# Optimization experiments

Hardware: AMD Instinct MI355X
Metric: run time of the kernel (lower is better)

Reference implementation:

```python
import jax, jax.numpy as jnp
import numpy as np

TOPK = 2

def setup_inputs() -> dict:
    key = jax.random.key(0)
    ks = jax.random.split(key, 5)
    B, S, D, H, E = 2, 4096, 1024, 2048, 8
    x = jax.random.normal(ks[0], (B, S, D), dtype=jnp.float32)
    router_w = jax.random.normal(ks[1], (E, D), dtype=jnp.float32) * 0.02
    w1 = jax.random.normal(ks[2], (E, D, H), dtype=jnp.float32) * 0.02
    w3 = jax.random.normal(ks[3], (E, D, H), dtype=jnp.float32) * 0.02
    w2 = jax.random.normal(ks[4], (E, H, D), dtype=jnp.float32) * 0.02
    return {"x": x, "router_w": router_w, "w1": w1, "w3": w3, "w2": w2}

def reference(x, router_w, w1, w3, w2):
    B, S, D = x.shape
    E = router_w.shape[0]
    xf = x.reshape(-1, D)                      # [T, D]
    T = xf.shape[0]
    logits = (xf @ router_w.T).astype(jnp.float32)      # [T, E]
    weights, indices = jax.lax.top_k(logits, TOPK)      # [T, k]
    weights = jax.nn.softmax(weights, axis=-1).astype(x.dtype)
    prob = jax.nn.softmax(logits, axis=-1)              # [T, E] fp32
    P = prob.mean(axis=0).astype(x.dtype)               # [E]
    mask = jnp.zeros((T, E), jnp.float32).at[jnp.arange(T)[:, None], indices].set(1.0)
    f = mask.mean(axis=0).astype(x.dtype)               # [E]
    aux_loss = E * jnp.sum(f * P)
    out = jnp.zeros_like(xf)
    for e in range(E):
        # combine weight for expert e per token (0 if not routed here)
        coef = jnp.sum(jnp.where(indices == e, weights, jnp.zeros_like(weights)), axis=-1)  # [T]
        h = jax.nn.silu(xf @ w1[e]) * (xf @ w3[e])      # [T, H] SwiGLU
        out = out + coef[:, None] * (h @ w2[e])         # masked combine == gather/scatter
    return out.reshape(B, S, D), aux_loss
```

## Files before the change

### kernel.cpp

```cpp
#include <hip/hip_runtime.h>
#include <hip/hip_bf16.h>

#define TT 8192
#define DD 1024
#define HH 2048
#define EE 8

typedef __bf16 bf16x8 __attribute__((ext_vector_type(8)));
typedef float floatx4 __attribute__((ext_vector_type(4)));
typedef short shortx8 __attribute__((ext_vector_type(8)));

__device__ __forceinline__ short f2bf(float f) {
  unsigned u = __float_as_uint(f);
  u += 0x7fffu + ((u >> 16) & 1u);
  return (short)(u >> 16);
}

__device__ __forceinline__ float bf2f(short s) {
  return __uint_as_float(((unsigned)(unsigned short)s) << 16);
}

__device__ __forceinline__ void gld16(const void* g, void* l) {
  __builtin_amdgcn_global_load_lds((const __attribute__((address_space(1))) void*)g,
                                   (__attribute__((address_space(3))) void*)l, 16, 0, 0);
}

__global__ __launch_bounds__(256) void prep_kernel(
    const float* __restrict__ x, const float* __restrict__ rw,
    const float* __restrict__ w1, const float* __restrict__ w3, const float* __restrict__ w2,
    int* __restrict__ cpad, float* __restrict__ ppad, int* __restrict__ ctr,
    int* __restrict__ offsets, float* __restrict__ out_aux,
    int* __restrict__ list_token, float* __restrict__ list_coef,
    int* __restrict__ tokpk, float* __restrict__ tokcf,
    short* __restrict__ xb, short* __restrict__ w13t, short* __restrict__ w2t)
{
  __shared__ short T[64 * 74];
  __shared__ int   sE0[32], sE1[32], lcnt[EE], sbase[EE], lp0[32], lp1[32];
  __shared__ float sG0[32], sG1[32], sP[EE];
  const int b = blockIdx.x;
  const int tid = threadIdx.x;

  if (b < 256) {
    if (tid < EE) { sP[tid] = 0.f; lcnt[tid] = 0; }
    __syncthreads();
    const int lane = tid & 63, wv = tid >> 6;
    const int t0 = b * 32;
    for (int ti = 0; ti < 8; ++ti) {
      const int s = wv * 8 + ti;
      const int t = t0 + s;
      float sc[EE];
#pragma unroll
      for (int e = 0; e < EE; ++e) sc[e] = 0.f;
#pragma unroll
      for (int j = 0; j < 4; ++j) {
        float4 xv = *(const float4*)(x + (size_t)t * DD + j * 256 + lane * 4);
#pragma unroll
        for (int e = 0; e < EE; ++e) {
          float4 rv = *(const float4*)(rw + e * DD + j * 256 + lane * 4);
          sc[e] += xv.x * rv.x + xv.y * rv.y + xv.z * rv.z + xv.w * rv.w;
        }
        if (xb) {
          short4 sv = make_short4(f2bf(xv.x), f2bf(xv.y), f2bf(xv.z), f2bf(xv.w));
          *(short4*)(xb + (size_t)t * DD + j * 256 + lane * 4) = sv;
        }
      }
#pragma unroll
      for (int off = 32; off > 0; off >>= 1)
#pragma unroll
        for (int e = 0; e < EE; ++e)
          sc[e] += __shfl_down(sc[e], off);
      if (lane == 0) {
        int i0 = 0; float l0 = sc[0];
        for (int e = 1; e < EE; ++e) if (sc[e] > l0) { l0 = sc[e]; i0 = e; }
        int i1 = -1; float l1 = -3.4e38f;
        for (int e = 0; e < EE; ++e) if (e != i0 && sc[e] > l1) { l1 = sc[e]; i1 = e; }
        const float g0 = 1.f / (1.f + __expf(l1 - l0));
        float pr[EE]; float sum = 0.f;
        for (int e = 0; e < EE; ++e) { pr[e] = __expf(sc[e] - l0); sum += pr[e]; }
        const float inv = 1.f / sum;
        for (int e = 0; e < EE; ++e) atomicAdd(&sP[e], pr[e] * inv);
        sE0[s] = i0; sE1[s] = i1; sG0[s] = g0; sG1[s] = 1.f - g0;
      }
    }
    __syncthreads();
    if (tid < 32) {
      lp0[tid] = atomicAdd(&lcnt[sE0[tid]], 1);
      lp1[tid] = atomicAdd(&lcnt[sE1[tid]], 1);
    }
    __syncthreads();
    if (tid < EE) {
      sbase[tid] = atomicAdd(&cpad[tid * 16], lcnt[tid]);
      atomicAdd(&ppad[tid * 16], sP[tid]);
    }
    __syncthreads();
    if (tid < 32) {
      int e0 = sE0[tid], e1 = sE1[tid], t = t0 + tid;
      int p0 = sbase[e0] + lp0[tid];
      int p1 = sbase[e1] + lp1[tid];
      list_token[e0 * TT + p0] = t; list_coef[e0 * TT + p0] = sG0[tid];
      list_token[e1 * TT + p1] = t; list_coef[e1 * TT + p1] = sG1[tid];
      tokpk[t * 2]     = (e0 << 13) | p0;  tokcf[t * 2]     = sG0[tid];
      tokpk[t * 2 + 1] = (e1 << 13) | p1;  tokcf[t * 2 + 1] = sG1[tid];
    }
    __syncthreads();
    if (tid == 0) {
      __threadfence();
      if (atomicAdd(ctr, 1) == 255) {
        float aux = 0.f; int off = 0;
        for (int e = 0; e < EE; ++e) {
          int c   = atomicAdd(&cpad[e * 16], 0);
          float p = atomicAdd(&ppad[e * 16], 0.f);
          aux += ((float)c / (float)TT) * (p / (float)TT);
          offsets[e] = off; off += c;
        }
        *out_aux = aux * (float)EE;
      }
    }
  } else if (b < 256 + 8192) {
    const int u = b - 256;
    const int xx = u & 31, yy = (u >> 5) & 15, z = u >> 9;
    const int is3 = (z >= EE) ? 1 : 0;
    const int e = is3 ? (z - EE) : z;
    const float* in = (is3 ? w3 : w1) + (size_t)e * DD * HH;
    short* o = w13t + (size_t)e * DD * HH * 2;
    const int c0 = xx * 64, r0 = yy * 64;
#pragma unroll
    for (int p = 0; p < 4; ++p) {
      int r = p * 16 + (tid >> 4), c4 = (tid & 15) * 4;
      float4 v = *(const float4*)(in + (size_t)(r0 + r) * HH + c0 + c4);
      short4 s = make_short4(f2bf(v.x), f2bf(v.y), f2bf(v.z), f2bf(v.w));
      *(short4*)&T[r * 74 + c4] = s;
    }
    __syncthreads();
#pragma unroll
    for (int q = 0; q < 2; ++q) {
      int uu = q * 256 + tid;
      int oc = uu >> 3, k8 = (uu & 7) * 8;
      shortx8 s;
#pragma unroll
      for (int j = 0; j < 8; ++j) s[j] = T[(k8 + j) * 74 + oc];
      int c = c0 + oc;
      int grow = 2 * (c & ~31) + (c & 31) + (is3 ? 32 : 0);
      *(shortx8*)&o[(size_t)grow * DD + r0 + k8] = s;
    }
  } else {
    const int v = b - 256 - 8192;
    const int xx = v & 15, yy = (v >> 4) & 31, z = v >> 9;
    const float* in = w2 + (size_t)z * HH * DD;
    short* o = w2t + (size_t)z * HH * DD;
    const int c0 = xx * 64, r0 = yy * 64;
#pragma unroll
    for (int p = 0; p < 4; ++p) {
      int r = p * 16 + (tid >> 4), c4 = (tid & 15) * 4;
      float4 vv = *(const float4*)(in + (size_t)(r0 + r) * DD + c0 + c4);
      short4 s = make_short4(f2bf(vv.x), f2bf(vv.y), f2bf(vv.z), f2bf(vv.w));
      *(short4*)&T[r * 74 + c4] = s;
    }
    __syncthreads();
#pragma unroll
    for (int q = 0; q < 2; ++q) {
      int uu = q * 256 + tid;
      int oc = uu >> 3, k8 = (uu & 7) * 8;
      shortx8 s;
#pragma unroll
      for (int j = 0; j < 8; ++j) s[j] = T[(k8 + j) * 74 + oc];
      *(shortx8*)&o[(size_t)(c0 + oc) * HH + r0 + k8] = s;
    }
  }
}

__global__ __launch_bounds__(256) void convt_kernel(const float* __restrict__ in, short* __restrict__ out,
                                                    int R, int C)
{
  __shared__ short T[64 * 74];
  const int t = threadIdx.x;
  in  += (size_t)blockIdx.z * R * C;
  out += (size_t)blockIdx.z * R * C;
  const int c0 = blockIdx.x * 64, r0 = blockIdx.y * 64;
#pragma unroll
  for (int p = 0; p < 4; ++p) {
    int r = p * 16 + (t >> 4), c4 = (t & 15) * 4;
    float4 v = *(const float4*)(in + (size_t)(r0 + r) * C + c0 + c4);
    short4 s = make_short4(f2bf(v.x), f2bf(v.y), f2bf(v.z), f2bf(v.w));
    *(short4*)&T[r * 74 + c4] = s;
  }
  __syncthreads();
#pragma unroll
  for (int q = 0; q < 2; ++q) {
    int u = q * 256 + t;
    int oc = u >> 3, k8 = (u & 7) * 8;
    shortx8 s;
#pragma unroll
    for (int j = 0; j < 8; ++j) s[j] = T[(k8 + j) * 74 + oc];
    *(shortx8*)&out[(size_t)(c0 + oc) * R + r0 + k8] = s;
  }
}


#define PH_BAR()  { __builtin_amdgcn_s_barrier(); __builtin_amdgcn_sched_barrier(0); }
#define WAITL0()  { asm volatile("s_waitcnt lgkmcnt(0)" ::: "memory"); __builtin_amdgcn_sched_barrier(0); }
#define WAITVN(n) { asm volatile("s_waitcnt vmcnt(" #n ")" ::: "memory"); __builtin_amdgcn_sched_barrier(0); }

template<int NT>
__device__ __forceinline__ void mma_core(char* SM, int tid,
    const char* a00, const char* a01, const char* a10, const char* a11,
    const char* b00, const char* b01, const char* b10, const char* b11,
    floatx4 (&acc)[8][4])
{
  const int lane = tid & 63, w = tid >> 6;
  const int l16 = lane & 15, quad = lane >> 4;
  const int wm = (w >> 2) & 1, wn = w & 3;
  const int cx = (((l16 >> 1) & 1) << 4) | (((l16 >> 2) & 1) << 5) | ((l16 & 1) << 6);
  const int ck0 = (quad * 16) ^ cx;
  const int arb = (wm * 128 + l16) * 128;
  const int brb = 32768 + (wn * 64 + l16) * 128;
  const int wq = w * 2048;

#define SA_(u,h,p0,p1) { gld16((p0) + (size_t)(u) * 128, SM + (((u) & 1) << 16) + (h) * 16384 + wq); \
                         gld16((p1) + (size_t)(u) * 128, SM + (((u) & 1) << 16) + (h) * 16384 + wq + 1024); }
#define SB_(u,h,p0,p1) { gld16((p0) + (size_t)(u) * 128, SM + (((u) & 1) << 16) + 32768 + (h) * 16384 + wq); \
                         gld16((p1) + (size_t)(u) * 128, SM + (((u) & 1) << 16) + 32768 + (h) * 16384 + wq + 1024); }
#define LA_(mi) { a[mi][0] = *(const bf16x8*)(SM + cur + arb + (mi) * 2048 + ck0); \
                  a[mi][1] = *(const bf16x8*)(SM + cur + arb + (mi) * 2048 + (ck0 ^ 64)); }
#define LB_(ni) { b[ni][0] = *(const bf16x8*)(SM + cur + brb + (ni) * 2048 + ck0); \
                  b[ni][1] = *(const bf16x8*)(SM + cur + brb + (ni) * 2048 + (ck0 ^ 64)); }
#define MM_(mi,ni) { acc[mi][ni] = __builtin_amdgcn_mfma_f32_16x16x32_bf16(a[mi][0], b[ni][0], acc[mi][ni], 0, 0, 0); \
                     acc[mi][ni] = __builtin_amdgcn_mfma_f32_16x16x32_bf16(a[mi][1], b[ni][1], acc[mi][ni], 0, 0, 0); }

  SA_(0, 0, a00, a01); SA_(0, 1, a10, a11);
  SB_(0, 0, b00, b01); SB_(0, 1, b10, b11);
  SA_(1, 0, a00, a01); SA_(1, 1, a10, a11);
  WAITVN(4);
  __builtin_amdgcn_s_barrier();
  __builtin_amdgcn_sched_barrier(0);

#pragma unroll 2
  for (int t = 0; t < NT; ++t) {
    const int cur = (t & 1) << 16;
    bf16x8 a[8][2], b[4][2];
    LA_(0) LA_(1) LA_(2) LA_(3) LB_(0) LB_(1)
    if (t + 1 < NT) SB_(t + 1, 0, b00, b01);
    PH_BAR(); WAITL0();
    __builtin_amdgcn_s_setprio(1);
    MM_(0,0) MM_(1,0) MM_(2,0) MM_(3,0) MM_(0,1) MM_(1,1) MM_(2,1) MM_(3,1)
    __builtin_amdgcn_s_setprio(0);
    PH_BAR();
    LA_(4) LA_(5) LA_(6) LA_(7) LB_(2) LB_(3)
    if (t + 1 < NT) SB_(t + 1, 1, b10, b11);
    PH_BAR(); WAITL0();
    __builtin_amdgcn_s_setprio(1);
    MM_(4,2) MM_(5,2) MM_(6,2) MM_(7,2) MM_(4,3) MM_(5,3) MM_(6,3) MM_(7,3)
    __builtin_amdgcn_s_setprio(0);
    PH_BAR();
    if (t + 2 < NT) SA_(t + 2, 0, a00, a01);
    PH_BAR();
    __builtin_amdgcn_s_setprio(1);
    MM_(0,2) MM_(1,2) MM_(2,2) MM_(3,2) MM_(0,3) MM_(1,3) MM_(2,3) MM_(3,3)
    __builtin_amdgcn_s_setprio(0);
    PH_BAR();
    if (t + 2 < NT) SA_(t + 2, 1, a10, a11);
    PH_BAR();
    __builtin_amdgcn_s_setprio(1);
    MM_(4,0) MM_(5,0) MM_(6,0) MM_(7,0) MM_(4,1) MM_(5,1) MM_(6,1) MM_(7,1)
    __builtin_amdgcn_s_setprio(0);
    if (t + 2 < NT) { WAITVN(4); } else { WAITVN(0); }
    PH_BAR();
  }
#undef SA_
#undef SB_
#undef LA_
#undef LB_
#undef MM_
}

__global__ __launch_bounds__(512, 2) void g1p_kernel(
    const short* __restrict__ xb, const short* __restrict__ w13t,
    const int* __restrict__ cpad, const int* __restrict__ offsets,
    const int* __restrict__ list_token, short* __restrict__ Hbuf)
{
  const int lin = blockIdx.x + 16 * (blockIdx.y + 32 * blockIdx.z);
  const int xcd = lin & 7, c = lin >> 3;
  const int e = c >> 6, rb = (c >> 1) & 31, nb = (xcd << 1) | (c & 1);
  const int cnt = cpad[e * 16];
  if (rb * 256 >= cnt) return;
  __shared__ char SM[131072];
  const int tid = threadIdx.x;
  const int lane = tid & 63, w = tid >> 6;
  const int srow = lane >> 3;
  const int scol = (((lane ^ (lane >> 4)) & 1) << 4)
                 | ((((lane >> 1) ^ (lane >> 5)) & 1) << 5)
                 | ((((lane >> 2) ^ (lane >> 3)) & 1) << 6);
  const int* lt = list_token + e * TT;
  const char* ap[2][2];
#pragma unroll
  for (int h = 0; h < 2; ++h)
#pragma unroll
    for (int i = 0; i < 2; ++i) {
      int gr = rb * 256 + h * 128 + (w * 2 + i) * 8 + srow;
      int tok = (gr < cnt) ? lt[gr] : lt[0];
      ap[h][i] = (const char*)xb + (size_t)tok * 2048 + scol;
    }
  const char* bb = (const char*)w13t + ((size_t)e * 4096 + nb * 256) * 2048
                 + (size_t)(w * 16 + srow) * 2048 + scol;
  floatx4 acc[8][4] = {};
  mma_core<16>(SM, tid, ap[0][0], ap[0][1], ap[1][0], ap[1][1],
               bb, bb + 8 * 2048, bb + 128 * 2048, bb + 136 * 2048, acc);
  const int off = offsets[e];
  const int l16 = lane & 15, quad = lane >> 4;
  const int wm = (w >> 2) & 1, wn = w & 3;
#pragma unroll
  for (int mi = 0; mi < 8; ++mi)
#pragma unroll
    for (int r = 0; r < 4; ++r) {
      int grow = rb * 256 + wm * 128 + mi * 16 + quad * 4 + r;
      if (grow < cnt) {
        size_t rowbase = (size_t)(off + grow) * HH + nb * 128 + wn * 32;
#pragma unroll
        for (int ni = 0; ni < 2; ++ni) {
          float aa = acc[mi][ni][r], bbv = acc[mi][ni + 2][r];
          float hv = aa / (1.f + __expf(-aa)) * bbv;
          Hbuf[rowbase + ni * 16 + l16] = f2bf(hv);
        }
      }
    }
}

__global__ __launch_bounds__(512, 2) void g2q_kernel(
    const short* __restrict__ Hbuf, const short* __restrict__ w2t,
    const int* __restrict__ cpad, const int* __restrict__ offsets,
    short* __restrict__ Obuf)
{
  const int nb = blockIdx.x, rb = blockIdx.y, e = blockIdx.z;
  const int cnt = cpad[e * 16];
  if (rb * 256 >= cnt) return;
  __shared__ char SM[131072];
  const int tid = threadIdx.x;
  const int lane = tid & 63, w = tid >> 6;
  const int srow = lane >> 3;
  const int scol = (((lane ^ (lane >> 4)) & 1) << 4)
                 | ((((lane >> 1) ^ (lane >> 5)) & 1) << 5)
                 | ((((lane >> 2) ^ (lane >> 3)) & 1) << 6);
  const int off = offsets[e];
  const char* ap[2][2];
#pragma unroll
  for (int h = 0; h < 2; ++h)
#pragma unroll
    for (int i = 0; i < 2; ++i) {
      int gr = rb * 256 + h * 128 + (w * 2 + i) * 8 + srow;
      int cg = (gr < cnt) ? gr : (cnt - 1);
      ap[h][i] = (const char*)Hbuf + (size_t)(off + cg) * 4096 + scol;
    }
  const char* bb = (const char*)w2t + ((size_t)e * DD + nb * 256) * 4096
                 + (size_t)(w * 16 + srow) * 4096 + scol;
  floatx4 acc[8][4] = {};
  mma_core<32>(SM, tid, ap[0][0], ap[0][1], ap[1][0], ap[1][1],
               bb, bb + 8 * 4096, bb + 128 * 4096, bb + 136 * 4096, acc);
  const int l16 = lane & 15, quad = lane >> 4;
  const int wm = (w >> 2) & 1, wn = w & 3;
#pragma unroll
  for (int mi = 0; mi < 8; ++mi)
#pragma unroll
    for (int r = 0; r < 4; ++r) {
      int grow = rb * 256 + wm * 128 + mi * 16 + quad * 4 + r;
      if (grow < cnt) {
        short* orow = Obuf + (size_t)(off + grow) * DD + nb * 256 + wn * 64;
#pragma unroll
        for (int ni = 0; ni < 4; ++ni)
          orow[ni * 16 + l16] = f2bf(acc[mi][ni][r]);
      }
    }
}

__global__ __launch_bounds__(256) void combine_kernel(
    const short* __restrict__ Obuf, const int* __restrict__ offsets,
    const int* __restrict__ tokpk, const float* __restrict__ tokcf,
    float* __restrict__ out)
{
  const int tid = threadIdx.x, lane = tid & 63, wv = tid >> 6;
  const int t = blockIdx.x * 4 + wv;
  const int pk0 = tokpk[t * 2], pk1 = tokpk[t * 2 + 1];
  const float c0 = tokcf[t * 2], c1 = tokcf[t * 2 + 1];
  const size_t r0 = (size_t)(offsets[pk0 >> 13] + (pk0 & 8191)) * DD;
  const size_t r1 = (size_t)(offsets[pk1 >> 13] + (pk1 & 8191)) * DD;
  float* orow = out + (size_t)t * DD;
#pragma unroll
  for (int p = 0; p < 2; ++p) {
    int cidx = p * 512 + lane * 8;
    shortx8 a = *(const shortx8*)(Obuf + r0 + cidx);
    shortx8 b = *(const shortx8*)(Obuf + r1 + cidx);
    float v[8];
#pragma unroll
    for (int j = 0; j < 8; ++j) v[j] = c0 * bf2f(a[j]) + c1 * bf2f(b[j]);
    *(float4*)(orow + cidx)     = make_float4(v[0], v[1], v[2], v[3]);
    *(float4*)(orow + cidx + 4) = make_float4(v[4], v[5], v[6], v[7]);
  }
}

__global__ __launch_bounds__(256, 2) void g1s_kernel(
    const float* __restrict__ x, const float* __restrict__ w1, const float* __restrict__ w3,
    const int* __restrict__ cpad, const int* __restrict__ offsets,
    const int* __restrict__ list_token, short* __restrict__ Hbuf)
{
  const int e = blockIdx.z, rb = blockIdx.y, nb = blockIdx.x;
  const int cnt = cpad[e * 16];
  if (rb * 128 >= cnt) return;
  __shared__ short Asm[128 * 40];
  __shared__ short B1sm[128 * 40];
  __shared__ short B3sm[128 * 40];
  const int tid = threadIdx.x, lane = tid & 63, wv = tid >> 6;
  const int wm = (wv >> 1) * 64, wn = (wv & 1) * 64;
  const int quad = lane >> 4, l16 = lane & 15;
  floatx4 acc1[4][4] = {{{0.f}}};
  floatx4 acc3[4][4] = {{{0.f}}};
  const int ar = tid >> 3, ak = (tid & 7) * 4;
  const int bp = tid & 63, bq = tid >> 6;
  const int bswz = (bq ^ ((bp >> 2) & 3)) * 8;
  const int bo0 = (2 * bp) * 40 + bswz, bo1 = bo0 + 40;
  int aro[4], bro[4];
#pragma unroll
  for (int mi = 0; mi < 4; ++mi) aro[mi] = (wm + mi * 16 + l16) * 40 + quad * 8;
#pragma unroll
  for (int ni = 0; ni < 4; ++ni) {
    int nl = wn + ni * 16 + l16;
    bro[ni] = nl * 40 + ((quad ^ ((nl >> 3) & 3)) * 8);
  }
  int tok[4];
#pragma unroll
  for (int i = 0; i < 4; ++i) {
    int gr = rb * 128 + ar + 32 * i;
    tok[i] = (gr < cnt) ? list_token[e * TT + gr] : list_token[e * TT];
  }
  const float* w1e = w1 + (size_t)e * DD * HH + (size_t)nb * 128;
  const float* w3e = w3 + (size_t)e * DD * HH + (size_t)nb * 128;
  for (int k0 = 0; k0 < DD; k0 += 32) {
    __syncthreads();
#pragma unroll
    for (int i = 0; i < 4; ++i) {
      int r = ar + 32 * i;
      float4 v = *(const float4*)(x + (size_t)tok[i] * DD + k0 + ak);
      short4 sv = make_short4(f2bf(v.x), f2bf(v.y), f2bf(v.z), f2bf(v.w));
      *(short4*)&Asm[r * 40 + ak] = sv;
    }
    {
      float2 u[8];
#pragma unroll
      for (int j = 0; j < 8; ++j) u[j] = *(const float2*)(w1e + (size_t)(k0 + bq * 8 + j) * HH + 2 * bp);
      shortx8 p0, p1;
#pragma unroll
      for (int j = 0; j < 8; ++j) { p0[j] = f2bf(u[j].x); p1[j] = f2bf(u[j].y); }
      *(shortx8*)&B1sm[bo0] = p0; *(shortx8*)&B1sm[bo1] = p1;
    }
    {
      float2 u[8];
#pragma unroll
      for (int j = 0; j < 8; ++j) u[j] = *(const float2*)(w3e + (size_t)(k0 + bq * 8 + j) * HH + 2 * bp);
      shortx8 p0, p1;
#pragma unroll
      for (int j = 0; j < 8; ++j) { p0[j] = f2bf(u[j].x); p1[j] = f2bf(u[j].y); }
      *(shortx8*)&B3sm[bo0] = p0; *(shortx8*)&B3sm[bo1] = p1;
    }
    __syncthreads();
    bf16x8 af[4], b1f[4], b3f[4];
#pragma unroll
    for (int mi = 0; mi < 4; ++mi) af[mi] = *(const bf16x8*)&Asm[aro[mi]];
#pragma unroll
    for (int ni = 0; ni < 4; ++ni) {
      b1f[ni] = *(const bf16x8*)&B1sm[bro[ni]];
      b3f[ni] = *(const bf16x8*)&B3sm[bro[ni]];
    }
#pragma unroll
    for (int mi = 0; mi < 4; ++mi)
#pragma unroll
      for (int ni = 0; ni < 4; ++ni) {
        acc1[mi][ni] = __builtin_amdgcn_mfma_f32_16x16x32_bf16(af[mi], b1f[ni], acc1[mi][ni], 0, 0, 0);
        acc3[mi][ni] = __builtin_amdgcn_mfma_f32_16x16x32_bf16(af[mi], b3f[ni], acc3[mi][ni], 0, 0, 0);
      }
  }
  const int off = offsets[e];
#pragma unroll
  for (int mi = 0; mi < 4; ++mi)
#pragma unroll
    for (int r = 0; r < 4; ++r) {
      int row = wm + mi * 16 + quad * 4 + r;
      int grow = rb * 128 + row;
      if (grow < cnt) {
        size_t rowbase = (size_t)(off + grow) * HH + (size_t)nb * 128 + wn;
#pragma unroll
        for (int ni = 0; ni < 4; ++ni) {
          float a = acc1[mi][ni][r], b = acc3[mi][ni][r];
          float h = a / (1.f + __expf(-a)) * b;
          Hbuf[rowbase + ni * 16 + l16] = f2bf(h);
        }
      }
    }
}

__global__ __launch_bounds__(256, 2) void g2s_kernel(
    const short* __restrict__ Hbuf, const float* __restrict__ w2,
    const int* __restrict__ cpad, const int* __restrict__ offsets,
    const int* __restrict__ list_token, const float* __restrict__ list_coef,
    float* __restrict__ out)
{
  const int e = blockIdx.z, rb = blockIdx.y, nb = blockIdx.x;
  const int cnt = cpad[e * 16];
  if (rb * 128 >= cnt) return;
  __shared__ short Asm[128 * 40];
  __shared__ short Bsm[128 * 40];
  const int tid = threadIdx.x, lane = tid & 63, wv = tid >> 6;
  const int wm = (wv >> 1) * 64, wn = (wv & 1) * 64;
  const int quad = lane >> 4, l16 = lane & 15;
  floatx4 acc[4][4] = {{{0.f}}};
  const int ar = tid >> 3, ak = (tid & 7) * 4;
  const int bp = tid & 63, bq = tid >> 6;
  const int bswz = (bq ^ ((bp >> 2) & 3)) * 8;
  const int bo0 = (2 * bp) * 40 + bswz, bo1 = bo0 + 40;
  int aro[4], bro[4];
#pragma unroll
  for (int mi = 0; mi < 4; ++mi) aro[mi] = (wm + mi * 16 + l16) * 40 + quad * 8;
#pragma unroll
  for (int ni = 0; ni < 4; ++ni) {
    int nl = wn + ni * 16 + l16;
    bro[ni] = nl * 40 + ((quad ^ ((nl >> 3) & 3)) * 8);
  }
  const int off = offsets[e];
  size_t hrow[4];
#pragma unroll
  for (int i = 0; i < 4; ++i) {
    int gr = rb * 128 + ar + 32 * i;
    int cg = (gr < cnt) ? gr : (cnt - 1);
    hrow[i] = (size_t)(off + cg) * HH;
  }
  const float* w2e = w2 + (size_t)e * HH * DD + (size_t)nb * 128;
  for (int k0 = 0; k0 < HH; k0 += 32) {
    __syncthreads();
#pragma unroll
    for (int i = 0; i < 4; ++i) {
      int r = ar + 32 * i;
      short4 sv = *(const short4*)(Hbuf + hrow[i] + k0 + ak);
      *(short4*)&Asm[r * 40 + ak] = sv;
    }
    {
      float2 u[8];
#pragma unroll
      for (int j = 0; j < 8; ++j) u[j] = *(const float2*)(w2e + (size_t)(k0 + bq * 8 + j) * DD + 2 * bp);
      shortx8 p0, p1;
#pragma unroll
      for (int j = 0; j < 8; ++j) { p0[j] = f2bf(u[j].x); p1[j] = f2bf(u[j].y); }
      *(shortx8*)&Bsm[bo0] = p0; *(shortx8*)&Bsm[bo1] = p1;
    }
    __syncthreads();
    bf16x8 af[4], bf[4];
#pragma unroll
    for (int mi = 0; mi < 4; ++mi) af[mi] = *(const bf16x8*)&Asm[aro[mi]];
#pragma unroll
    for (int ni = 0; ni < 4; ++ni) bf[ni] = *(const bf16x8*)&Bsm[bro[ni]];
#pragma unroll
    for (int mi = 0; mi < 4; ++mi)
#pragma unroll
      for (int ni = 0; ni < 4; ++ni)
        acc[mi][ni] = __builtin_amdgcn_mfma_f32_16x16x32_bf16(af[mi], bf[ni], acc[mi][ni], 0, 0, 0);
  }
#pragma unroll
  for (int mi = 0; mi < 4; ++mi)
#pragma unroll
    for (int r = 0; r < 4; ++r) {
      int row = wm + mi * 16 + quad * 4 + r;
      int grow = rb * 128 + row;
      if (grow < cnt) {
        int tokid = list_token[e * TT + grow];
        float coef = list_coef[e * TT + grow];
        float* orow = out + (size_t)tokid * DD + (size_t)nb * 128 + wn;
#pragma unroll
        for (int ni = 0; ni < 4; ++ni)
          atomicAdd(&orow[ni * 16 + l16], coef * acc[mi][ni][r]);
      }
    }
}

extern "C" void kernel_launch(void* const* d_in, const int* in_sizes, int n_in,
                              void* d_out, int out_size, void* d_ws, size_t ws_size,
                              hipStream_t stream)
{
  const float* x  = (const float*)d_in[0];
  const float* rw = (const float*)d_in[1];
  const float* w1 = (const float*)d_in[2];
  const float* w3 = (const float*)d_in[3];
  const float* w2 = (const float*)d_in[4];
  float* out = (float*)d_out;

  char* ws = (char*)d_ws;
  int*   cpad      = (int*)(ws + 0);
  float* ppad      = (float*)(ws + 512);
  int*   offsets   = (int*)(ws + 1024);
  int*   ctr       = (int*)(ws + 2048);
  int*   list_tok  = (int*)(ws + 4096);
  float* list_coef = (float*)(ws + 4096 + EE * TT * 4);
  int*   tokpk     = (int*)(ws + 4096 + 2 * EE * TT * 4);
  float* tokcf     = (float*)(ws + 4096 + 2 * EE * TT * 4 + 2 * TT * 4);

  const size_t OFF_W1T = 1u << 20;
  const size_t OFF_W3T = OFF_W1T + ((size_t)EE * DD * HH * 2);
  const size_t OFF_XBF = OFF_W3T + ((size_t)EE * DD * HH * 2);
  const size_t OFF_HB  = OFF_XBF + ((size_t)TT * DD * 2);
  const size_t NEED    = OFF_HB + ((size_t)(2 * TT + 128) * HH * 2);
  const size_t OFF_W2T = NEED;
  const size_t NEED2   = NEED + ((size_t)EE * DD * HH * 2);

  hipMemsetAsync(ws, 0, 4096, stream);

  const bool fast  = (ws_size >= NEED);
  const bool tier2 = (ws_size >= NEED2);
  short* XBF = fast ? (short*)(ws + OFF_XBF) : nullptr;

  if (fast) {
    short* W13T = (short*)(ws + OFF_W1T);
    short* OB   = (short*)(ws + OFF_W1T);
    short* W2T  = tier2 ? (short*)(ws + OFF_W2T) : (short*)(ws + OFF_W3T);
    short* HB   = (short*)(ws + OFF_HB);
    const int nblk = 256 + 8192 + (tier2 ? 4096 : 0);
    prep_kernel<<<nblk, 256, 0, stream>>>(x, rw, w1, w3, w2, cpad, ppad, ctr, offsets,
                                          out + (size_t)TT * DD, list_tok, list_coef,
                                          tokpk, tokcf, XBF, W13T, W2T);
    g1p_kernel<<<dim3(16, 32, EE), 512, 0, stream>>>(XBF, W13T, cpad, offsets, list_tok, HB);
    if (!tier2)
      convt_kernel<<<dim3(DD / 64, HH / 64, EE), 256, 0, stream>>>(w2, W2T, HH, DD);
    g2q_kernel<<<dim3(DD / 256, 32, EE), 512, 0, stream>>>(HB, W2T, cpad, offsets, OB);
    combine_kernel<<<TT / 4, 256, 0, stream>>>(OB, offsets, tokpk, tokcf, out);
  } else {
    hipMemsetAsync(d_out, 0, (size_t)TT * DD * sizeof(float), stream);
    short* HB = (short*)(ws + (1 << 20));
    prep_kernel<<<256, 256, 0, stream>>>(x, rw, w1, w3, w2, cpad, ppad, ctr, offsets,
                                         out + (size_t)TT * DD, list_tok, list_coef,
                                         tokpk, tokcf, nullptr, nullptr, nullptr);
    g1s_kernel<<<dim3(HH / 128, TT / 128, EE), 256, 0, stream>>>(x, w1, w3, cpad, offsets, list_tok, HB);
    g2s_kernel<<<dim3(DD / 128, TT / 128, EE), 256, 0, stream>>>(HB, w2, cpad, offsets, list_tok, list_coef, out);
  }
}
```

Measured before the change: 578.2 us.

## Restructure MFMA main loop to prefetch next-tile A fragments and cut barriers

Reorganizes the double-buffered GEMM inner loop so that the first half of the A fragments for the next K-tile is read from LDS into registers during the current tile's MFMA phases. B loads for the next tile are issued together, and most of the per-phase workgroup barriers are removed, leaving two per iteration. The aim is to overlap LDS reads and global-to-LDS copies with matrix math and to cut barrier stalls. In exchange, register fragments stay live across iterations, and the buffer-hazard ordering now depends on fewer waitcnt/barrier points, which risks races and higher register pressure.

```diff
diff --git a/kernel.cpp b/kernel.cpp
--- a/kernel.cpp
+++ b/kernel.cpp
@@ -209,11 +209,11 @@
 {
   const int lane = tid & 63, w = tid >> 6;
   const int l16 = lane & 15, quad = lane >> 4;
-  const int wm = (w >> 2) & 1, wn = w & 3;
   const int cx = (((l16 >> 1) & 1) << 4) | (((l16 >> 2) & 1) << 5) | ((l16 & 1) << 6);
   const int ck0 = (quad * 16) ^ cx;
+  const int wm = (w >> 2) & 1;
   const int arb = (wm * 128 + l16) * 128;
-  const int brb = 32768 + (wn * 64 + l16) * 128;
+  const int brb = 32768 + ((w & 3) * 64 + l16) * 128;
   const int wq = w * 2048;
 
 #define SA_(u,h,p0,p1) { gld16((p0) + (size_t)(u) * 128, SM + (((u) & 1) << 16) + (h) * 16384 + wq); \
@@ -222,10 +222,14 @@
                          gld16((p1) + (size_t)(u) * 128, SM + (((u) & 1) << 16) + 32768 + (h) * 16384 + wq + 1024); }
 #define LA_(mi) { a[mi][0] = *(const bf16x8*)(SM + cur + arb + (mi) * 2048 + ck0); \
                   a[mi][1] = *(const bf16x8*)(SM + cur + arb + (mi) * 2048 + (ck0 ^ 64)); }
+#define LAo_(mi) { a[mi][0] = *(const bf16x8*)(SM + oth + arb + (mi) * 2048 + ck0); \
+                   a[mi][1] = *(const bf16x8*)(SM + oth + arb + (mi) * 2048 + (ck0 ^ 64)); }
 #define LB_(ni) { b[ni][0] = *(const bf16x8*)(SM + cur + brb + (ni) * 2048 + ck0); \
                   b[ni][1] = *(const bf16x8*)(SM + cur + brb + (ni) * 2048 + (ck0 ^ 64)); }
 #define MM_(mi,ni) { acc[mi][ni] = __builtin_amdgcn_mfma_f32_16x16x32_bf16(a[mi][0], b[ni][0], acc[mi][ni], 0, 0, 0); \
                      acc[mi][ni] = __builtin_amdgcn_mfma_f32_16x16x32_bf16(a[mi][1], b[ni][1], acc[mi][ni], 0, 0, 0); }
+
+  bf16x8 a[8][2], b[4][2];
 
   SA_(0, 0, a00, a01); SA_(0, 1, a10, a11);
   SB_(0, 0, b00, b01); SB_(0, 1, b10, b11);
@@ -233,42 +237,48 @@
   WAITVN(4);
   __builtin_amdgcn_s_barrier();
   __builtin_amdgcn_sched_barrier(0);
+  {
+    const int cur = 0;
+    LA_(0) LA_(1) LA_(2) LA_(3)
+  }
+  __builtin_amdgcn_sched_barrier(0);
 
 #pragma unroll 2
   for (int t = 0; t < NT; ++t) {
     const int cur = (t & 1) << 16;
-    bf16x8 a[8][2], b[4][2];
-    LA_(0) LA_(1) LA_(2) LA_(3) LB_(0) LB_(1)
-    if (t + 1 < NT) SB_(t + 1, 0, b00, b01);
-    PH_BAR(); WAITL0();
+    const int oth = cur ^ (1 << 16);
+    LB_(0) LB_(1)
+    LA_(4) LA_(5) LA_(6) LA_(7)
+    LB_(2) LB_(3)
     __builtin_amdgcn_s_setprio(1);
     MM_(0,0) MM_(1,0) MM_(2,0) MM_(3,0) MM_(0,1) MM_(1,1) MM_(2,1) MM_(3,1)
     __builtin_amdgcn_s_setprio(0);
+    __builtin_amdgcn_sched_barrier(0);
+    if (t + 1 < NT) { SB_(t + 1, 0, b00, b01); SB_(t + 1, 1, b10, b11); }
+    __builtin_amdgcn_s_setprio(1);
+    MM_(0,2) MM_(1,2) MM_(2,2) MM_(3,2) MM_(0,3) MM_(1,3) MM_(2,3) MM_(3,3)
+    __builtin_amdgcn_s_setprio(0);
+    WAITL0();
     PH_BAR();
-    LA_(4) LA_(5) LA_(6) LA_(7) LB_(2) LB_(3)
-    if (t + 1 < NT) SB_(t + 1, 1, b10, b11);
-    PH_BAR(); WAITL0();
+    WAITVN(4);
+    if (t + 2 < NT) SA_(t + 2, 0, a00, a01);
+    if (t + 1 < NT) { LAo_(0) LAo_(1) LAo_(2) LAo_(3) }
     __builtin_amdgcn_s_setprio(1);
     MM_(4,2) MM_(5,2) MM_(6,2) MM_(7,2) MM_(4,3) MM_(5,3) MM_(6,3) MM_(7,3)
     __builtin_amdgcn_s_setprio(0);
-    PH_BAR();
-    if (t + 2 < NT) SA_(t + 2, 0, a00, a01);
-    PH_BAR();
-    __builtin_amdgcn_s_setprio(1);
-    MM_(0,2) MM_(1,2) MM_(2,2) MM_(3,2) MM_(0,3) MM_(1,3) MM_(2,3) MM_(3,3)
-    __builtin_amdgcn_s_setprio(0);
-    PH_BAR();
+    __builtin_amdgcn_sched_barrier(0);
     if (t + 2 < NT) SA_(t + 2, 1, a10, a11);
-    PH_BAR();
     __builtin_amdgcn_s_setprio(1);
     MM_(4,0) MM_(5,0) MM_(6,0) MM_(7,0) MM_(4,1) MM_(5,1) MM_(6,1) MM_(7,1)
     __builtin_amdgcn_s_setprio(0);
+    WAITL0();
     if (t + 2 < NT) { WAITVN(4); } else { WAITVN(0); }
     PH_BAR();
   }
 #undef SA_
 #undef SB_
 #undef LA_
+#undef LAo_
 #undef LB_
 #undef MM_
 }
```

After: 574.1 us (median of 2 runs). No clear change (-0.7%).

## Use 16-wave 1024-thread blocks with 64x64 per-wave MFMA tiles in expert GEMMs

Applied to the files above, without the earlier changes.

Both expert GEMM kernels move from 8 waves per block, each computing a 128x64 sub-tile, to 16 waves per block arranged 4x4, each computing a 64x64 sub-tile. The 256x256 block tile is unchanged. The intent is to cut per-wave accumulator and fragment registers and put more waves in flight to hide latency. The main loop becomes simpler: two K-halves, each with LDS fragment loads then 16 MFMAs. The finely interleaved global-to-LDS prefetch between compute phases is dropped, and the next stage's A and B loads are issued together after compute, which loses some load/compute overlap. The launch bounds of (1024, 4) may also force a tight VGPR budget and cause spills.

```diff
diff --git a/kernel.cpp b/kernel.cpp
--- a/kernel.cpp
+++ b/kernel.cpp
@@ -202,34 +202,45 @@
 #define WAITVN(n) { asm volatile("s_waitcnt vmcnt(" #n ")" ::: "memory"); __builtin_amdgcn_sched_barrier(0); }
 
 template<int NT>
-__device__ __forceinline__ void mma_core(char* SM, int tid,
-    const char* a00, const char* a01, const char* a10, const char* a11,
-    const char* b00, const char* b01, const char* b10, const char* b11,
-    floatx4 (&acc)[8][4])
+__device__ __forceinline__ void mma_core16(char* SM, int tid,
+    const char* a0, const char* a1, const char* b0, const char* b1,
+    floatx4 (&acc)[4][4])
 {
   const int lane = tid & 63, w = tid >> 6;
   const int l16 = lane & 15, quad = lane >> 4;
-  const int wm = (w >> 2) & 1, wn = w & 3;
   const int cx = (((l16 >> 1) & 1) << 4) | (((l16 >> 2) & 1) << 5) | ((l16 & 1) << 6);
   const int ck0 = (quad * 16) ^ cx;
-  const int arb = (wm * 128 + l16) * 128;
+  const int wm = w >> 2, wn = w & 3;
+  const int arb = (wm * 64 + l16) * 128;
   const int brb = 32768 + (wn * 64 + l16) * 128;
   const int wq = w * 2048;
 
-#define SA_(u,h,p0,p1) { gld16((p0) + (size_t)(u) * 128, SM + (((u) & 1) << 16) + (h) * 16384 + wq); \
-                         gld16((p1) + (size_t)(u) * 128, SM + (((u) & 1) << 16) + (h) * 16384 + wq + 1024); }
-#define SB_(u,h,p0,p1) { gld16((p0) + (size_t)(u) * 128, SM + (((u) & 1) << 16) + 32768 + (h) * 16384 + wq); \
-                         gld16((p1) + (size_t)(u) * 128, SM + (((u) & 1) << 16) + 32768 + (h) * 16384 + wq + 1024); }
-#define LA_(mi) { a[mi][0] = *(const bf16x8*)(SM + cur + arb + (mi) * 2048 + ck0); \
-                  a[mi][1] = *(const bf16x8*)(SM + cur + arb + (mi) * 2048 + (ck0 ^ 64)); }
-#define LB_(ni) { b[ni][0] = *(const bf16x8*)(SM + cur + brb + (ni) * 2048 + ck0); \
-                  b[ni][1] = *(const bf16x8*)(SM + cur + brb + (ni) * 2048 + (ck0 ^ 64)); }
-#define MM_(mi,ni) { acc[mi][ni] = __builtin_amdgcn_mfma_f32_16x16x32_bf16(a[mi][0], b[ni][0], acc[mi][ni], 0, 0, 0); \
-                     acc[mi][ni] = __builtin_amdgcn_mfma_f32_16x16x32_bf16(a[mi][1], b[ni][1], acc[mi][ni], 0, 0, 0); }
-
-  SA_(0, 0, a00, a01); SA_(0, 1, a10, a11);
-  SB_(0, 0, b00, b01); SB_(0, 1, b10, b11);
-  SA_(1, 0, a00, a01); SA_(1, 1, a10, a11);
+#define SA_(u) { gld16(a0 + (size_t)(u) * 128, SM + (((u) & 1) << 16) + wq); \
+                 gld16(a1 + (size_t)(u) * 128, SM + (((u) & 1) << 16) + wq + 1024); }
+#define SB_(u) { gld16(b0 + (size_t)(u) * 128, SM + (((u) & 1) << 16) + 32768 + wq); \
+                 gld16(b1 + (size_t)(u) * 128, SM + (((u) & 1) << 16) + 32768 + wq + 1024); }
+#define LA_(mi,kk) { a[mi] = *(const bf16x8*)(SM + cur + arb + (mi) * 2048 + (ck0 ^ (kk))); }
+#define LB_(ni,kk) { b[ni] = *(const bf16x8*)(SM + cur + brb + (ni) * 2048 + (ck0 ^ (kk))); }
+#define MM16() { \
+  acc[0][0] = __builtin_amdgcn_mfma_f32_16x16x32_bf16(a[0], b[0], acc[0][0], 0, 0, 0); \
+  acc[1][0] = __builtin_amdgcn_mfma_f32_16x16x32_bf16(a[1], b[0], acc[1][0], 0, 0, 0); \
+  acc[2][0] = __builtin_amdgcn_mfma_f32_16x16x32_bf16(a[2], b[0], acc[2][0], 0, 0, 0); \
+  acc[3][0] = __builtin_amdgcn_mfma_f32_16x16x32_bf16(a[3], b[0], acc[3][0], 0, 0, 0); \
+  acc[0][1] = __builtin_amdgcn_mfma_f32_16x16x32_bf16(a[0], b[1], acc[0][1], 0, 0, 0); \
+  acc[1][1] = __builtin_amdgcn_mfma_f32_16x16x32_bf16(a[1], b[1], acc[1][1], 0, 0, 0); \
+  acc[2][1] = __builtin_amdgcn_mfma_f32_16x16x32_bf16(a[2], b[1], acc[2][1], 0, 0, 0); \
+  acc[3][1] = __builtin_amdgcn_mfma_f32_16x16x32_bf16(a[3], b[1], acc[3][1], 0, 0, 0); \
+  acc[0][2] = __builtin_amdgcn_mfma_f32_16x16x32_bf16(a[0], b[2], acc[0][2], 0, 0, 0); \
+  acc[1][2] = __builtin_amdgcn_mfma_f32_16x16x32_bf16(a[1], b[2], acc[1][2], 0, 0, 0); \
+  acc[2][2] = __builtin_amdgcn_mfma_f32_16x16x32_bf16(a[2], b[2], acc[2][2], 0, 0, 0); \
+  acc[3][2] = __builtin_amdgcn_mfma_f32_16x16x32_bf16(a[3], b[2], acc[3][2], 0, 0, 0); \
+  acc[0][3] = __builtin_amdgcn_mfma_f32_16x16x32_bf16(a[0], b[3], acc[0][3], 0, 0, 0); \
+  acc[1][3] = __builtin_amdgcn_mfma_f32_16x16x32_bf16(a[1], b[3], acc[1][3], 0, 0, 0); \
+  acc[2][3] = __builtin_amdgcn_mfma_f32_16x16x32_bf16(a[2], b[3], acc[2][3], 0, 0, 0); \
+  acc[3][3] = __builtin_amdgcn_mfma_f32_16x16x32_bf16(a[3], b[3], acc[3][3], 0, 0, 0); }
+
+  SA_(0); SB_(0);
+  SA_(1); SB_(1);
   WAITVN(4);
   __builtin_amdgcn_s_barrier();
   __builtin_amdgcn_sched_barrier(0);
@@ -237,32 +248,22 @@
 #pragma unroll 2
   for (int t = 0; t < NT; ++t) {
     const int cur = (t & 1) << 16;
-    bf16x8 a[8][2], b[4][2];
-    LA_(0) LA_(1) LA_(2) LA_(3) LB_(0) LB_(1)
-    if (t + 1 < NT) SB_(t + 1, 0, b00, b01);
-    PH_BAR(); WAITL0();
+    bf16x8 a[4], b[4];
+    LA_(0, 0) LA_(1, 0) LA_(2, 0) LA_(3, 0)
+    LB_(0, 0) LB_(1, 0) LB_(2, 0) LB_(3, 0)
+    WAITL0();
     __builtin_amdgcn_s_setprio(1);
-    MM_(0,0) MM_(1,0) MM_(2,0) MM_(3,0) MM_(0,1) MM_(1,1) MM_(2,1) MM_(3,1)
+    MM16();
+    __builtin_amdgcn_s_setprio(0);
+    __builtin_amdgcn_sched_barrier(0);
+    LA_(0, 64) LA_(1, 64) LA_(2, 64) LA_(3, 64)
+    LB_(0, 64) LB_(1, 64) LB_(2, 64) LB_(3, 64)
+    WAITL0();
+    __builtin_amdgcn_s_setprio(1);
+    MM16();
     __builtin_amdgcn_s_setprio(0);
     PH_BAR();
-    LA_(4) LA_(5) LA_(6) LA_(7) LB_(2) LB_(3)
-    if (t + 1 < NT) SB_(t + 1, 1, b10, b11);
-    PH_BAR(); WAITL0();
-    __builtin_amdgcn_s_setprio(1);
-    MM_(4,2) MM_(5,2) MM_(6,2) MM_(7,2) MM_(4,3) MM_(5,3) MM_(6,3) MM_(7,3)
-    __builtin_amdgcn_s_setprio(0);
-    PH_BAR();
-    if (t + 2 < NT) SA_(t + 2, 0, a00, a01);
-    PH_BAR();
-    __builtin_amdgcn_s_setprio(1);
-    MM_(0,2) MM_(1,2) MM_(2,2) MM_(3,2) MM_(0,3) MM_(1,3) MM_(2,3) MM_(3,3)
-    __builtin_amdgcn_s_setprio(0);
-    PH_BAR();
-    if (t + 2 < NT) SA_(t + 2, 1, a10, a11);
-    PH_BAR();
-    __builtin_amdgcn_s_setprio(1);
-    MM_(4,0) MM_(5,0) MM_(6,0) MM_(7,0) MM_(4,1) MM_(5,1) MM_(6,1) MM_(7,1)
-    __builtin_amdgcn_s_setprio(0);
+    if (t + 2 < NT) { SA_(t + 2); SB_(t + 2); }
     if (t + 2 < NT) { WAITVN(4); } else { WAITVN(0); }
     PH_BAR();
   }
@@ -270,10 +271,10 @@
 #undef SB_
 #undef LA_
 #undef LB_
-#undef MM_
-}
-
-__global__ __launch_bounds__(512, 2) void g1p_kernel(
+#undef MM16
+}
+
+__global__ __launch_bounds__(1024, 4) void g1p_kernel(
     const short* __restrict__ xb, const short* __restrict__ w13t,
     const int* __restrict__ cpad, const int* __restrict__ offsets,
     const int* __restrict__ list_token, short* __restrict__ Hbuf)
@@ -291,28 +292,29 @@
                  | ((((lane >> 1) ^ (lane >> 5)) & 1) << 5)
                  | ((((lane >> 2) ^ (lane >> 3)) & 1) << 6);
   const int* lt = list_token + e * TT;
-  const char* ap[2][2];
-#pragma unroll
-  for (int h = 0; h < 2; ++h)
-#pragma unroll
-    for (int i = 0; i < 2; ++i) {
-      int gr = rb * 256 + h * 128 + (w * 2 + i) * 8 + srow;
-      int tok = (gr < cnt) ? lt[gr] : lt[0];
-      ap[h][i] = (const char*)xb + (size_t)tok * 2048 + scol;
-    }
-  const char* bb = (const char*)w13t + ((size_t)e * 4096 + nb * 256) * 2048
-                 + (size_t)(w * 16 + srow) * 2048 + scol;
-  floatx4 acc[8][4] = {};
-  mma_core<16>(SM, tid, ap[0][0], ap[0][1], ap[1][0], ap[1][1],
-               bb, bb + 8 * 2048, bb + 128 * 2048, bb + 136 * 2048, acc);
+  const char* ap[2];
+#pragma unroll
+  for (int i = 0; i < 2; ++i) {
+    int gr = rb * 256 + w * 16 + i * 8 + srow;
+    int tok = (gr < cnt) ? lt[gr] : lt[0];
+    ap[i] = (const char*)xb + (size_t)tok * 2048 + scol;
+  }
+  const char* bp[2];
+#pragma unroll
+  for (int i = 0; i < 2; ++i) {
+    int brow = nb * 256 + w * 16 + i * 8 + srow;
+    bp[i] = (const char*)w13t + ((size_t)e * 4096 + brow) * 2048 + scol;
+  }
+  floatx4 acc[4][4] = {};
+  mma_core16<16>(SM, tid, ap[0], ap[1], bp[0], bp[1], acc);
   const int off = offsets[e];
   const int l16 = lane & 15, quad = lane >> 4;
-  const int wm = (w >> 2) & 1, wn = w & 3;
-#pragma unroll
-  for (int mi = 0; mi < 8; ++mi)
+  const int wm = w >> 2, wn = w & 3;
+#pragma unroll
+  for (int mi = 0; mi < 4; ++mi)
 #pragma unroll
     for (int r = 0; r < 4; ++r) {
-      int grow = rb * 256 + wm * 128 + mi * 16 + quad * 4 + r;
+      int grow = rb * 256 + wm * 64 + mi * 16 + quad * 4 + r;
       if (grow < cnt) {
         size_t rowbase = (size_t)(off + grow) * HH + nb * 128 + wn * 32;
 #pragma unroll
@@ -325,7 +327,7 @@
     }
 }
 
-__global__ __launch_bounds__(512, 2) void g2q_kernel(
+__global__ __launch_bounds__(1024, 4) void g2q_kernel(
     const short* __restrict__ Hbuf, const short* __restrict__ w2t,
     const int* __restrict__ cpad, const int* __restrict__ offsets,
     short* __restrict__ Obuf)
@@ -341,27 +343,28 @@
                  | ((((lane >> 1) ^ (lane >> 5)) & 1) << 5)
                  | ((((lane >> 2) ^ (lane >> 3)) & 1) << 6);
   const int off = offsets[e];
-  const char* ap[2][2];
-#pragma unroll
-  for (int h = 0; h < 2; ++h)
-#pragma unroll
-    for (int i = 0; i < 2; ++i) {
-      int gr = rb * 256 + h * 128 + (w * 2 + i) * 8 + srow;
-      int cg = (gr < cnt) ? gr : (cnt - 1);
-      ap[h][i] = (const char*)Hbuf + (size_t)(off + cg) * 4096 + scol;
-    }
-  const char* bb = (const char*)w2t + ((size_t)e * DD + nb * 256) * 4096
-                 + (size_t)(w * 16 + srow) * 4096 + scol;
-  floatx4 acc[8][4] = {};
-  mma_core<32>(SM, tid, ap[0][0], ap[0][1], ap[1][0], ap[1][1],
-               bb, bb + 8 * 4096, bb + 128 * 4096, bb + 136 * 4096, acc);
+  const char* ap[2];
+#pragma unroll
+  for (int i = 0; i < 2; ++i) {
+    int gr = rb * 256 + w * 16 + i * 8 + srow;
+    int cg = (gr < cnt) ? gr : (cnt - 1);
+    ap[i] = (const char*)Hbuf + (size_t)(off + cg) * 4096 + scol;
+  }
+  const char* bp[2];
+#pragma unroll
+  for (int i = 0; i < 2; ++i) {
+    int brow = nb * 256 + w * 16 + i * 8 + srow;
+    bp[i] = (const char*)w2t + ((size_t)e * DD + brow) * 4096 + scol;
+  }
+  floatx4 acc[4][4] = {};
+  mma_core16<32>(SM, tid, ap[0], ap[1], bp[0], bp[1], acc);
   const int l16 = lane & 15, quad = lane >> 4;
-  const int wm = (w >> 2) & 1, wn = w & 3;
-#pragma unroll
-  for (int mi = 0; mi < 8; ++mi)
+  const int wm = w >> 2, wn = w & 3;
+#pragma unroll
+  for (int mi = 0; mi < 4; ++mi)
 #pragma unroll
     for (int r = 0; r < 4; ++r) {
-      int grow = rb * 256 + wm * 128 + mi * 16 + quad * 4 + r;
+      int grow = rb * 256 + wm * 64 + mi * 16 + quad * 4 + r;
       if (grow < cnt) {
         short* orow = Obuf + (size_t)(off + grow) * DD + nb * 256 + wn * 64;
 #pragma unroll
@@ -621,10 +624,10 @@
     prep_kernel<<<nblk, 256, 0, stream>>>(x, rw, w1, w3, w2, cpad, ppad, ctr, offsets,
                                           out + (size_t)TT * DD, list_tok, list_coef,
                                           tokpk, tokcf, XBF, W13T, W2T);
-    g1p_kernel<<<dim3(16, 32, EE), 512, 0, stream>>>(XBF, W13T, cpad, offsets, list_tok, HB);
+    g1p_kernel<<<dim3(16, 32, EE), 1024, 0, stream>>>(XBF, W13T, cpad, offsets, list_tok, HB);
     if (!tier2)
       convt_kernel<<<dim3(DD / 64, HH / 64, EE), 256, 0, stream>>>(w2, W2T, HH, DD);
-    g2q_kernel<<<dim3(DD / 256, 32, EE), 512, 0, stream>>>(HB, W2T, cpad, offsets, OB);
+    g2q_kernel<<<dim3(DD / 256, 32, EE), 1024, 0, stream>>>(HB, W2T, cpad, offsets, OB);
     combine_kernel<<<TT / 4, 256, 0, stream>>>(OB, offsets, tokpk, tokcf, out);
   } else {
     hipMemsetAsync(d_out, 0, (size_t)TT * DD * sizeof(float), stream);
```

Result: slower. 602.5 us (+4.2%).
